# Performance work log

Measured on AMD Instinct MI355X. Metric: run time of the kernel, lower is better.

Reference implementation:

```python
import jax, jax.numpy as jnp
import numpy as np

D_MODEL = 768
N_HEADS = 12
D_K = D_MODEL // N_HEADS
LORA_RANK = 8
LORA_ALPHA = 16
SCALING = LORA_ALPHA / LORA_RANK  # lora scaling = alpha / rank
SCALE = float(np.sqrt(D_K))      # attention scale = sqrt(d_k)


def setup_inputs() -> dict:
    key = jax.random.key(0)
    ks = jax.random.split(key, 16)
    s = 0.02
    inp = {
        "x": jax.random.normal(ks[0], (1, 4096, D_MODEL), dtype=jnp.float32),
        # base projections: torch Linear weights are [out, in]
        "wq": jax.random.normal(ks[1], (D_MODEL, D_MODEL), dtype=jnp.float32) * s,
        "bq": jax.random.normal(ks[2], (D_MODEL,), dtype=jnp.float32) * s,
        "wk": jax.random.normal(ks[3], (D_MODEL, D_MODEL), dtype=jnp.float32) * s,
        "bk": jax.random.normal(ks[4], (D_MODEL,), dtype=jnp.float32) * s,
        "wv": jax.random.normal(ks[5], (D_MODEL, D_MODEL), dtype=jnp.float32) * s,
        "bv": jax.random.normal(ks[6], (D_MODEL,), dtype=jnp.float32) * s,
        "wo": jax.random.normal(ks[7], (D_MODEL, D_MODEL), dtype=jnp.float32) * s,
        "bo": jax.random.normal(ks[8], (D_MODEL,), dtype=jnp.float32) * s,
        # LoRA adapters (no bias): down [rank, d_model], up [d_model, rank]
        "wq_down": jax.random.normal(ks[9], (LORA_RANK, D_MODEL), dtype=jnp.float32) * s,
        "wq_up": jax.random.normal(ks[10], (D_MODEL, LORA_RANK), dtype=jnp.float32) * s,
        "wk_down": jax.random.normal(ks[11], (LORA_RANK, D_MODEL), dtype=jnp.float32) * s,
        "wk_up": jax.random.normal(ks[12], (D_MODEL, LORA_RANK), dtype=jnp.float32) * s,
        "wv_down": jax.random.normal(ks[13], (LORA_RANK, D_MODEL), dtype=jnp.float32) * s,
        "wv_up": jax.random.normal(ks[14], (D_MODEL, LORA_RANK), dtype=jnp.float32) * s,
    }
    return inp


def _lora_proj(x, w, b, w_down, w_up):
    # base Linear + scaled LoRA path (dropout = identity at inference)
    base = jnp.einsum("bsd,ed->bse", x, w) + b
    lora = jnp.einsum("bsr,er->bse", jnp.einsum("bsd,rd->bsr", x, w_down), w_up)
    return base + lora * SCALING


def reference(x, wq, bq, wk, bk, wv, bv, wo, bo,
              wq_down, wq_up, wk_down, wk_up, wv_down, wv_up):
    b, s, _ = x.shape
    q = _lora_proj(x, wq, bq, wq_down, wq_up)
    k = _lora_proj(x, wk, bk, wk_down, wk_up)
    v = _lora_proj(x, wv, bv, wv_down, wv_up)
    # [b, h, s, d_k]
    q = q.reshape(b, s, N_HEADS, D_K).transpose(0, 2, 1, 3)
    k = k.reshape(b, s, N_HEADS, D_K).transpose(0, 2, 1, 3)
    v = v.reshape(b, s, N_HEADS, D_K).transpose(0, 2, 1, 3)
    scores = jnp.einsum("bhqd,bhkd->bhqk", q, k) / SCALE
    probs = jax.nn.softmax(scores, axis=-1)
    attn = jnp.einsum("bhqk,bhkd->bhqd", probs, v)
    attn = attn.transpose(0, 2, 1, 3).reshape(b, s, D_MODEL)
    return jnp.einsum("bsd,ed->bse", attn, wo) + bo
```

## Files before the change

kernel.cpp:

```cpp
#include <hip/hip_runtime.h>

typedef unsigned short u16;
typedef __attribute__((ext_vector_type(8))) short short8;
typedef __attribute__((ext_vector_type(4))) float f32x4;
typedef __attribute__((ext_vector_type(4))) unsigned short u16x4;

typedef __attribute__((address_space(1))) void as1_void;
typedef __attribute__((address_space(3))) void as3_void;

__device__ __forceinline__ void gld16(const u16* g, u16* l) {
  __builtin_amdgcn_global_load_lds((as1_void*)g, (as3_void*)l, 16, 0, 0);
}

__device__ __forceinline__ u16 f2bf(float f) {
  unsigned u = __float_as_uint(f);
  u += 0x7fffu + ((u >> 16) & 1u);
  return (u16)(u >> 16);
}

__global__ void prep_all(const float* __restrict__ x, u16* __restrict__ xb,
                         const float* __restrict__ wq, const float* __restrict__ wk, const float* __restrict__ wv,
                         const float* __restrict__ dq, const float* __restrict__ uq,
                         const float* __restrict__ dk, const float* __restrict__ uk,
                         const float* __restrict__ dv, const float* __restrict__ uv,
                         const float* __restrict__ wo, u16* __restrict__ weff, u16* __restrict__ wob) {
  int bid = blockIdx.x;
  if (bid < 3072) {
    int i = bid * 256 + threadIdx.x;
    f32x4 f = *(const f32x4*)(x + (size_t)i * 4);
    u16x4 o;
#pragma unroll
    for (int r = 0; r < 4; ++r) o[r] = f2bf(f[r]);
    *(u16x4*)(xb + (size_t)i * 4) = o;
    return;
  }
  int idx = (bid - 3072) * 256 + threadIdx.x;
  int n = idx / 768, d = idx - n * 768;
  if (n >= 2304) {
    wob[(n - 2304) * 768 + d] = f2bf(wo[(n - 2304) * 768 + d]);
    return;
  }
  const float *w, *dn, *up; int e;
  if (n < 768)       { w = wq; dn = dq; up = uq; e = n; }
  else if (n < 1536) { w = wk; dn = dk; up = uk; e = n - 768; }
  else               { w = wv; dn = dv; up = uv; e = n - 1536; }
  float acc = w[e * 768 + d];
  float lo = 0.f;
#pragma unroll
  for (int r = 0; r < 8; ++r) lo += up[e * 8 + r] * dn[r * 768 + d];
  weff[idx] = f2bf(acc + 2.0f * lo);
}

template <int MT>
__global__ __launch_bounds__(256) void gemm_nt(
    const u16* __restrict__ A, const u16* __restrict__ B, int K, int mode,
    const float* __restrict__ bq, const float* __restrict__ bk, const float* __restrict__ bv,
    u16* __restrict__ qo, u16* __restrict__ ko, u16* __restrict__ vto,
    const float* __restrict__ bo, float* __restrict__ fo) {
  constexpr int TI = (MT == 128) ? 4 : 2;
  constexpr int TJ = (MT == 128) ? 4 : 2;
  __shared__ u16 As[MT * 32];
  __shared__ u16 Bs[128 * 32];
  const int tid = threadIdx.x;
  const int lane = tid & 63;
  const int wid = tid >> 6;
  const int qd = lane >> 4;
  const int m16 = lane & 15;
  const int rowbase = (MT == 128) ? (wid >> 1) * 64 : 0;
  const int colbase = (MT == 128) ? (wid & 1) * 64 : wid * 32;
  const int m0 = blockIdx.x * MT, n0 = blockIdx.y * 128;

  f32x4 acc[TI][TJ];
#pragma unroll
  for (int i = 0; i < TI; ++i)
#pragma unroll
    for (int j = 0; j < TJ; ++j)
#pragma unroll
      for (int e = 0; e < 4; ++e) acc[i][j][e] = 0.f;

  for (int k0 = 0; k0 < K; k0 += 32) {
    __syncthreads();
#pragma unroll
    for (int p = tid; p < MT * 4; p += 256) {
      int row = p >> 2;
      int g = (p & 3) ^ ((row >> 1) & 3);
      gld16(A + (size_t)(m0 + row) * K + k0 + g * 8, &As[(p - lane) * 8]);
    }
#pragma unroll
    for (int p = tid; p < 512; p += 256) {
      int row = p >> 2;
      int g = (p & 3) ^ ((row >> 1) & 3);
      gld16(B + (size_t)(n0 + row) * K + k0 + g * 8, &Bs[(p - lane) * 8]);
    }
    __syncthreads();
    short8 af[TI], bf[TJ];
#pragma unroll
    for (int i = 0; i < TI; ++i) {
      int ar = rowbase + i * 16 + m16;
      af[i] = *(const short8*)&As[(ar * 4 + (qd ^ ((ar >> 1) & 3))) * 8];
    }
#pragma unroll
    for (int j = 0; j < TJ; ++j) {
      int br = colbase + j * 16 + m16;
      bf[j] = *(const short8*)&Bs[(br * 4 + (qd ^ ((br >> 1) & 3))) * 8];
    }
#pragma unroll
    for (int i = 0; i < TI; ++i)
#pragma unroll
      for (int j = 0; j < TJ; ++j)
        acc[i][j] = __builtin_amdgcn_mfma_f32_16x16x32_bf16(af[i], bf[j], acc[i][j], 0, 0, 0);
  }

#pragma unroll
  for (int i = 0; i < TI; ++i) {
    int gr = m0 + rowbase + i * 16 + qd * 4;
#pragma unroll
    for (int j = 0; j < TJ; ++j) {
      int gc = n0 + colbase + j * 16 + m16;
      if (mode == 0) {
        if (gc < 768) {
          float bias = bq[gc];
          int h = gc >> 6, d = gc & 63;
#pragma unroll
          for (int r = 0; r < 4; ++r)
            qo[((size_t)h * 4096 + gr + r) * 64 + d] = f2bf((acc[i][j][r] + bias) * 0.18033688f);
        } else if (gc < 1536) {
          int c = gc - 768;
          float bias = bk[c];
          int h = c >> 6, d = c & 63;
#pragma unroll
          for (int r = 0; r < 4; ++r)
            ko[((size_t)h * 4096 + gr + r) * 64 + d] = f2bf(acc[i][j][r] + bias);
        } else {
          int c = gc - 1536;
          float bias = bv[c];
          int h = c >> 6, d = c & 63;
          u16x4 pk;
#pragma unroll
          for (int r = 0; r < 4; ++r) pk[r] = f2bf(acc[i][j][r] + bias);
          *(u16x4*)&vto[((size_t)h * 64 + d) * 4096 + gr] = pk;
        }
      } else {
        float bias = bo[gc];
#pragma unroll
        for (int r = 0; r < 4; ++r)
          fo[(size_t)(gr + r) * 768 + gc] = acc[i][j][r] + bias;
      }
    }
  }
}

__global__ __launch_bounds__(256) void attn_fwd(
    const u16* __restrict__ Q, const u16* __restrict__ Kg, const u16* __restrict__ Vt,
    float* __restrict__ Opart, float* __restrict__ lpart, u16* __restrict__ abo, int kspl) {
  __shared__ u16 Ks[2][64 * 64];
  __shared__ u16 Vs[2][64 * 64];
  __shared__ u16 Ps[16 * 640];
  const int tid = threadIdx.x, lane = tid & 63, wid = tid >> 6;
  const int qd = lane >> 4, m16 = lane & 15;
  const int h = blockIdx.y;
  const int qrow = blockIdx.x * 256 + wid * 64;
  const int kbase = blockIdx.z * (4096 / kspl);
  const int niter = (4096 / kspl) >> 6;

  short8 qf[4][2];
#pragma unroll
  for (int t = 0; t < 4; ++t) {
    const u16* qb = Q + ((size_t)h * 4096 + qrow + t * 16 + m16) * 64;
    qf[t][0] = *(const short8*)(qb + qd * 8);
    qf[t][1] = *(const short8*)(qb + 32 + qd * 8);
  }

  float lrun[4] = {0.f, 0.f, 0.f, 0.f};
  f32x4 oacc[4][4];
#pragma unroll
  for (int t = 0; t < 4; ++t)
#pragma unroll
    for (int d = 0; d < 4; ++d)
#pragma unroll
      for (int r = 0; r < 4; ++r) oacc[t][d][r] = 0.f;

  u16* pw = &Ps[wid * 4 * 640];
  const u16* kgh = Kg + (size_t)h * 4096 * 64;
  const u16* vth = Vt + (size_t)h * 64 * 4096;

  {
    const int kt = kbase;
#pragma unroll
    for (int rr = 0; rr < 2; ++rr) {
      int p = rr * 256 + tid;
      int row = p >> 3;
      int g = (p & 7) ^ (row & 7);
      gld16(kgh + (size_t)(kt + row) * 64 + g * 8, &Ks[0][(p - lane) * 8]);
      gld16(vth + (size_t)row * 4096 + kt + g * 8, &Vs[0][(p - lane) * 8]);
    }
  }

  for (int it = 0; it < niter; ++it) {
    __syncthreads();
    if (it + 1 < niter) {
      const int kt = kbase + (it + 1) * 64;
      const int b = (it + 1) & 1;
#pragma unroll
      for (int rr = 0; rr < 2; ++rr) {
        int p = rr * 256 + tid;
        int row = p >> 3;
        int g = (p & 7) ^ (row & 7);
        gld16(kgh + (size_t)(kt + row) * 64 + g * 8, &Ks[b][(p - lane) * 8]);
        gld16(vth + (size_t)row * 4096 + kt + g * 8, &Vs[b][(p - lane) * 8]);
      }
    }
    const u16* ks = Ks[it & 1];
    const u16* vs = Vs[it & 1];

#pragma unroll
    for (int qq = 0; qq < 2; ++qq) {
#pragma unroll
      for (int c2 = 0; c2 < 2; ++c2) {
        int c = qq * 2 + c2;
        int kr = c * 16 + m16;
        short8 kf0 = *(const short8*)&ks[(kr * 8 + (qd ^ (kr & 7))) * 8];
        short8 kf1 = *(const short8*)&ks[(kr * 8 + ((4 + qd) ^ (kr & 7))) * 8];
#pragma unroll
        for (int t = 0; t < 4; ++t) {
          f32x4 s = {0.f, 0.f, 0.f, 0.f};
          s = __builtin_amdgcn_mfma_f32_16x16x32_bf16(kf0, qf[t][0], s, 0, 0, 0);
          s = __builtin_amdgcn_mfma_f32_16x16x32_bf16(kf1, qf[t][1], s, 0, 0, 0);
          u16x4 pk;
          float lp = 0.f;
#pragma unroll
          for (int r = 0; r < 4; ++r) {
            float p = __builtin_amdgcn_exp2f(s[r]);
            lp += p;
            pk[r] = (u16)((__float_as_uint(p) + 0x8000u) >> 16);
          }
          lrun[t] += lp;
          *(u16x4*)&pw[t * 640 + m16 * 40 + c2 * 16 + qd * 4] = pk;
        }
      }
      short8 pf[4];
#pragma unroll
      for (int t = 0; t < 4; ++t)
        pf[t] = *(const short8*)&pw[t * 640 + m16 * 40 + qd * 8];
#pragma unroll
      for (int d = 0; d < 4; ++d) {
        int vr = d * 16 + m16;
        int g = qq * 4 + qd;
        short8 vf = *(const short8*)&vs[(vr * 8 + (g ^ (vr & 7))) * 8];
#pragma unroll
        for (int t = 0; t < 4; ++t)
          oacc[t][d] = __builtin_amdgcn_mfma_f32_16x16x32_bf16(pf[t], vf, oacc[t][d], 0, 0, 0);
      }
    }
  }

#pragma unroll
  for (int t = 0; t < 4; ++t) {
    lrun[t] += __shfl_xor(lrun[t], 16);
    lrun[t] += __shfl_xor(lrun[t], 32);
  }

  if (kspl > 1) {
#pragma unroll
    for (int t = 0; t < 4; ++t)
      if (lane < 16)
        lpart[((size_t)blockIdx.z * 4096 + qrow + t * 16 + m16) * 12 + h] = lrun[t];
    float* ob = Opart + (size_t)blockIdx.z * 4096 * 768;
#pragma unroll
    for (int t = 0; t < 4; ++t)
#pragma unroll
      for (int d = 0; d < 4; ++d)
#pragma unroll
        for (int r = 0; r < 4; ++r)
          ob[(size_t)(qrow + t * 16 + qd * 4 + r) * 768 + h * 64 + d * 16 + m16] = oacc[t][d][r];
  } else {
#pragma unroll
    for (int t = 0; t < 4; ++t) {
      float li[4];
#pragma unroll
      for (int r = 0; r < 4; ++r) li[r] = 1.0f / __shfl(lrun[t], qd * 4 + r);
#pragma unroll
      for (int d = 0; d < 4; ++d)
#pragma unroll
        for (int r = 0; r < 4; ++r)
          abo[(size_t)(qrow + t * 16 + qd * 4 + r) * 768 + h * 64 + d * 16 + m16] =
              f2bf(oacc[t][d][r] * li[r]);
    }
  }
}

__global__ void merge_norm(const float* __restrict__ Opart, const float* __restrict__ lpart,
                           u16* __restrict__ abo, int ksp) {
  int i = blockIdx.x * 256 + threadIdx.x;
  int s = i / 192, cq = i - s * 192;
  int h = cq >> 4;
  f32x4 a = {0.f, 0.f, 0.f, 0.f};
  float l = 0.f;
  for (int z = 0; z < ksp; ++z) {
    f32x4 b = *(const f32x4*)(Opart + (size_t)z * 4096 * 768 + (size_t)i * 4);
#pragma unroll
    for (int r = 0; r < 4; ++r) a[r] += b[r];
    l += lpart[((size_t)z * 4096 + s) * 12 + h];
  }
  float rl = 1.0f / l;
  u16x4 o;
#pragma unroll
  for (int r = 0; r < 4; ++r) o[r] = f2bf(a[r] * rl);
  *(u16x4*)(abo + (size_t)i * 4) = o;
}

extern "C" void kernel_launch(void* const* d_in, const int* in_sizes, int n_in,
                              void* d_out, int out_size, void* d_ws, size_t ws_size,
                              hipStream_t stream) {
  const float* x   = (const float*)d_in[0];
  const float* wq  = (const float*)d_in[1];
  const float* bq  = (const float*)d_in[2];
  const float* wk  = (const float*)d_in[3];
  const float* bk  = (const float*)d_in[4];
  const float* wv  = (const float*)d_in[5];
  const float* bv  = (const float*)d_in[6];
  const float* wo  = (const float*)d_in[7];
  const float* bo  = (const float*)d_in[8];
  const float* dq  = (const float*)d_in[9];
  const float* uq  = (const float*)d_in[10];
  const float* dk  = (const float*)d_in[11];
  const float* uk  = (const float*)d_in[12];
  const float* dv  = (const float*)d_in[13];
  const float* uv  = (const float*)d_in[14];
  float* out = (float*)d_out;

  char* ws = (char*)d_ws;
  u16* xb    = (u16*)(ws);
  u16* ab    = (u16*)(ws);
  u16* weff  = (u16*)(ws + 6291456);
  u16* wob   = (u16*)(ws + 9830400);
  u16* qb    = (u16*)(ws + 11010048);
  u16* kb    = (u16*)(ws + 17301504);
  u16* vtb   = (u16*)(ws + 23592960);
  float* Op  = (float*)(ws + 29884416);
  float* lp  = (float*)(ws + 80216064);

  int kspl = 1;
  if (ws_size >= 81002496ull) kspl = 4;
  else if (ws_size >= 55443456ull) {
    kspl = 2;
    lp = (float*)(ws + 55050240);
  }

  prep_all<<<12288, 256, 0, stream>>>(x, xb, wq, wk, wv, dq, uq, dk, uk, dv, uv, wo, weff, wob);
  gemm_nt<128><<<dim3(32, 18), 256, 0, stream>>>(xb, weff, 768, 0, bq, bk, bv, qb, kb, vtb,
                                                 nullptr, nullptr);
  attn_fwd<<<dim3(16, 12, kspl), 256, 0, stream>>>(qb, kb, vtb, Op, lp, ab, kspl);
  if (kspl > 1) merge_norm<<<3072, 256, 0, stream>>>(Op, lp, ab, kspl);
  gemm_nt<32><<<dim3(128, 6), 256, 0, stream>>>(ab, wob, 768, 1, nullptr, nullptr, nullptr,
                                                nullptr, nullptr, nullptr, bo, out);
}
```

Baseline: 235.4 us.

## Switch attention to 32x32x16 MFMA with register-resident P via permlane32 swap

Rewrites the attention inner loop to use 32x32x16 bf16 MFMA tiles instead of 16x16x32. The P matrix is rearranged into the A-operand layout in registers using v_cvt_pk_bf16_f32 and permlane32_swap, which removes the LDS round-trip and the Ps shared buffer. The aim is fewer LDS writes and reads and fewer MFMA issues per tile. In exchange, the output and row-sum indexing is more intricate and the larger accumulators may raise register pressure.

```diff
diff --git a/kernel.cpp b/kernel.cpp
--- a/kernel.cpp
+++ b/kernel.cpp
@@ -3,7 +3,9 @@
 typedef unsigned short u16;
 typedef __attribute__((ext_vector_type(8))) short short8;
 typedef __attribute__((ext_vector_type(4))) float f32x4;
+typedef __attribute__((ext_vector_type(16))) float f32x16;
 typedef __attribute__((ext_vector_type(4))) unsigned short u16x4;
+typedef __attribute__((ext_vector_type(2))) unsigned int uint2v;
 
 typedef __attribute__((address_space(1))) void as1_void;
 typedef __attribute__((address_space(3))) void as3_void;
@@ -16,6 +18,12 @@
   unsigned u = __float_as_uint(f);
   u += 0x7fffu + ((u >> 16) & 1u);
   return (u16)(u >> 16);
+}
+
+__device__ __forceinline__ short8 mk8(unsigned a, unsigned b, unsigned c, unsigned d) {
+  union { unsigned u[4]; short8 s; } x;
+  x.u[0] = a; x.u[1] = b; x.u[2] = c; x.u[3] = d;
+  return x.s;
 }
 
 __global__ void prep_all(const float* __restrict__ x, u16* __restrict__ xb,
@@ -155,32 +163,30 @@
     float* __restrict__ Opart, float* __restrict__ lpart, u16* __restrict__ abo, int kspl) {
   __shared__ u16 Ks[2][64 * 64];
   __shared__ u16 Vs[2][64 * 64];
-  __shared__ u16 Ps[16 * 640];
   const int tid = threadIdx.x, lane = tid & 63, wid = tid >> 6;
-  const int qd = lane >> 4, m16 = lane & 15;
+  const int q32 = lane & 31, hf = lane >> 5;
   const int h = blockIdx.y;
   const int qrow = blockIdx.x * 256 + wid * 64;
   const int kbase = blockIdx.z * (4096 / kspl);
   const int niter = (4096 / kspl) >> 6;
 
-  short8 qf[4][2];
-#pragma unroll
-  for (int t = 0; t < 4; ++t) {
-    const u16* qb = Q + ((size_t)h * 4096 + qrow + t * 16 + m16) * 64;
-    qf[t][0] = *(const short8*)(qb + qd * 8);
-    qf[t][1] = *(const short8*)(qb + 32 + qd * 8);
-  }
-
-  float lrun[4] = {0.f, 0.f, 0.f, 0.f};
-  f32x4 oacc[4][4];
-#pragma unroll
-  for (int t = 0; t < 4; ++t)
-#pragma unroll
-    for (int d = 0; d < 4; ++d)
-#pragma unroll
-      for (int r = 0; r < 4; ++r) oacc[t][d][r] = 0.f;
-
-  u16* pw = &Ps[wid * 4 * 640];
+  short8 qf[2][4];
+#pragma unroll
+  for (int t = 0; t < 2; ++t) {
+    const u16* qb = Q + ((size_t)h * 4096 + qrow + 32 * t + q32) * 64 + hf * 8;
+#pragma unroll
+    for (int ds = 0; ds < 4; ++ds) qf[t][ds] = *(const short8*)(qb + ds * 16);
+  }
+
+  float lrun[2] = {0.f, 0.f};
+  f32x16 oacc[2][2];
+#pragma unroll
+  for (int t = 0; t < 2; ++t)
+#pragma unroll
+    for (int d = 0; d < 2; ++d)
+#pragma unroll
+      for (int r = 0; r < 16; ++r) oacc[t][d][r] = 0.f;
+
   const u16* kgh = Kg + (size_t)h * 4096 * 64;
   const u16* vth = Vt + (size_t)h * 64 * 4096;
 
@@ -214,77 +220,86 @@
     const u16* vs = Vs[it & 1];
 
 #pragma unroll
-    for (int qq = 0; qq < 2; ++qq) {
-#pragma unroll
-      for (int c2 = 0; c2 < 2; ++c2) {
-        int c = qq * 2 + c2;
-        int kr = c * 16 + m16;
-        short8 kf0 = *(const short8*)&ks[(kr * 8 + (qd ^ (kr & 7))) * 8];
-        short8 kf1 = *(const short8*)&ks[(kr * 8 + ((4 + qd) ^ (kr & 7))) * 8];
-#pragma unroll
-        for (int t = 0; t < 4; ++t) {
-          f32x4 s = {0.f, 0.f, 0.f, 0.f};
-          s = __builtin_amdgcn_mfma_f32_16x16x32_bf16(kf0, qf[t][0], s, 0, 0, 0);
-          s = __builtin_amdgcn_mfma_f32_16x16x32_bf16(kf1, qf[t][1], s, 0, 0, 0);
-          u16x4 pk;
-          float lp = 0.f;
-#pragma unroll
-          for (int r = 0; r < 4; ++r) {
-            float p = __builtin_amdgcn_exp2f(s[r]);
-            lp += p;
-            pk[r] = (u16)((__float_as_uint(p) + 0x8000u) >> 16);
-          }
-          lrun[t] += lp;
-          *(u16x4*)&pw[t * 640 + m16 * 40 + c2 * 16 + qd * 4] = pk;
+    for (int kst = 0; kst < 2; ++kst) {
+      const int krow = kst * 32 + q32;
+      short8 kf[4];
+#pragma unroll
+      for (int ds = 0; ds < 4; ++ds) {
+        int c = ds * 2 + hf;
+        kf[ds] = *(const short8*)&ks[((krow << 3) + (c ^ (krow & 7))) * 8];
+      }
+      short8 pa[2][2];
+#pragma unroll
+      for (int t = 0; t < 2; ++t) {
+        f32x16 s;
+#pragma unroll
+        for (int r = 0; r < 16; ++r) s[r] = 0.f;
+#pragma unroll
+        for (int ds = 0; ds < 4; ++ds)
+          s = __builtin_amdgcn_mfma_f32_32x32x16_bf16(kf[ds], qf[t][ds], s, 0, 0, 0);
+        unsigned w[8];
+        float ls = 0.f;
+#pragma unroll
+        for (int i = 0; i < 8; ++i) {
+          float p0 = __builtin_amdgcn_exp2f(s[2 * i]);
+          float p1 = __builtin_amdgcn_exp2f(s[2 * i + 1]);
+          ls += p0 + p1;
+          asm("v_cvt_pk_bf16_f32 %0, %1, %2" : "=v"(w[i]) : "v"(p0), "v"(p1));
         }
-      }
-      short8 pf[4];
-#pragma unroll
-      for (int t = 0; t < 4; ++t)
-        pf[t] = *(const short8*)&pw[t * 640 + m16 * 40 + qd * 8];
-#pragma unroll
-      for (int d = 0; d < 4; ++d) {
-        int vr = d * 16 + m16;
-        int g = qq * 4 + qd;
-        short8 vf = *(const short8*)&vs[(vr * 8 + (g ^ (vr & 7))) * 8];
-#pragma unroll
-        for (int t = 0; t < 4; ++t)
-          oacc[t][d] = __builtin_amdgcn_mfma_f32_16x16x32_bf16(pf[t], vf, oacc[t][d], 0, 0, 0);
-      }
-    }
-  }
-
-#pragma unroll
-  for (int t = 0; t < 4; ++t) {
-    lrun[t] += __shfl_xor(lrun[t], 16);
-    lrun[t] += __shfl_xor(lrun[t], 32);
-  }
+        lrun[t] += ls;
+        uint2v r0 = __builtin_amdgcn_permlane32_swap(w[0], w[2], false, false);
+        uint2v r1 = __builtin_amdgcn_permlane32_swap(w[1], w[3], false, false);
+        uint2v r2 = __builtin_amdgcn_permlane32_swap(w[4], w[6], false, false);
+        uint2v r3 = __builtin_amdgcn_permlane32_swap(w[5], w[7], false, false);
+        pa[t][0] = mk8(r0[0], r1[0], r0[1], r1[1]);
+        pa[t][1] = mk8(r2[0], r3[0], r2[1], r3[1]);
+      }
+#pragma unroll
+      for (int dt = 0; dt < 2; ++dt) {
+        const int vrow = dt * 32 + q32;
+#pragma unroll
+        for (int ksl = 0; ksl < 2; ++ksl) {
+          int c = kst * 4 + ksl * 2 + hf;
+          short8 vf = *(const short8*)&vs[((vrow << 3) + (c ^ (vrow & 7))) * 8];
+#pragma unroll
+          for (int t = 0; t < 2; ++t)
+            oacc[t][dt] = __builtin_amdgcn_mfma_f32_32x32x16_bf16(pa[t][ksl], vf, oacc[t][dt], 0, 0, 0);
+        }
+      }
+    }
+  }
+
+#pragma unroll
+  for (int t = 0; t < 2; ++t) lrun[t] += __shfl_xor(lrun[t], 32);
 
   if (kspl > 1) {
 #pragma unroll
-    for (int t = 0; t < 4; ++t)
-      if (lane < 16)
-        lpart[((size_t)blockIdx.z * 4096 + qrow + t * 16 + m16) * 12 + h] = lrun[t];
+    for (int t = 0; t < 2; ++t)
+      if (hf == 0)
+        lpart[((size_t)blockIdx.z * 4096 + qrow + 32 * t + q32) * 12 + h] = lrun[t];
     float* ob = Opart + (size_t)blockIdx.z * 4096 * 768;
 #pragma unroll
-    for (int t = 0; t < 4; ++t)
-#pragma unroll
-      for (int d = 0; d < 4; ++d)
-#pragma unroll
-        for (int r = 0; r < 4; ++r)
-          ob[(size_t)(qrow + t * 16 + qd * 4 + r) * 768 + h * 64 + d * 16 + m16] = oacc[t][d][r];
+    for (int t = 0; t < 2; ++t)
+#pragma unroll
+      for (int r = 0; r < 16; ++r) {
+        int qloc = (r & 3) + 8 * (r >> 2) + 4 * hf;
+#pragma unroll
+        for (int dt = 0; dt < 2; ++dt)
+          ob[(size_t)(qrow + 32 * t + qloc) * 768 + h * 64 + dt * 32 + q32] = oacc[t][dt][r];
+      }
   } else {
 #pragma unroll
-    for (int t = 0; t < 4; ++t) {
-      float li[4];
-#pragma unroll
-      for (int r = 0; r < 4; ++r) li[r] = 1.0f / __shfl(lrun[t], qd * 4 + r);
-#pragma unroll
-      for (int d = 0; d < 4; ++d)
-#pragma unroll
-        for (int r = 0; r < 4; ++r)
-          abo[(size_t)(qrow + t * 16 + qd * 4 + r) * 768 + h * 64 + d * 16 + m16] =
-              f2bf(oacc[t][d][r] * li[r]);
+    for (int t = 0; t < 2; ++t) {
+      float linv = 1.0f / lrun[t];
+#pragma unroll
+      for (int r = 0; r < 16; ++r) {
+        int qloc = (r & 3) + 8 * (r >> 2) + 4 * hf;
+        float li = __shfl(linv, qloc);
+#pragma unroll
+        for (int dt = 0; dt < 2; ++dt)
+          abo[(size_t)(qrow + 32 * t + qloc) * 768 + h * 64 + dt * 32 + q32] =
+              f2bf(oacc[t][dt][r] * li);
+      }
     }
   }
 }
```

Result: no change. 237.9 us (+1.1%).
